# Kernel optimization log

Measured on AMD Instinct MI355X. Metric: run time of the kernel, lower is better.

## Reference

```python
import jax, jax.numpy as jnp
import numpy as np

N, C, H, W = 16, 64, 128, 128
SHIFT = 1  # frozen value of torch module's random.randint(-2, 2) drawn at __init__


def setup_inputs() -> dict:
    key = jax.random.key(0)
    k1, k2, k3 = jax.random.split(key, 3)
    x = jax.random.normal(k1, (N, C, H, W), dtype=jnp.float32)
    # p_3: Conv2d(c, c, (1,5), padding=(0,2), bias=False) -> weight (C_out, C_in, 1, 5)
    w3 = jax.random.normal(k2, (C, C, 1, 5), dtype=jnp.float32) * (1.0 / np.sqrt(5.0 * C))
    # p_7: Conv2d(9c, c, 1, groups=c, bias=False) -> per output channel, 9 input channels: (C, 9)
    w7 = jax.random.normal(k3, (C, 9), dtype=jnp.float32) * (1.0 / 3.0)
    return {"x": x, "w3": w3, "w7": w7}


def reference(x, w3, w7):
    n, c, h, w = x.shape
    # t_1: F.unfold(x, (1,3), dilation=(1,2), padding=(0,2)) -> width offsets -2, 0, +2 (zero padded)
    xp = jnp.pad(x, ((0, 0), (0, 0), (0, 0), (2, 2)))
    t1 = jnp.stack([xp[..., 0:w], xp[..., 2:w + 2], xp[..., 4:w + 4]], axis=2)  # (n,c,3,h,w)
    # t_3: 1x5 conv, padding (0,2)
    t3 = jax.lax.conv_general_dilated(
        x, w3, window_strides=(1, 1), padding=[(0, 0), (2, 2)],
        dimension_numbers=("NCHW", "OIHW", "NCHW"))  # (n,c,h,w)
    # t_4: F.unfold(t1 as (n,3c,h,w), (3,1), padding=(1,0)) -> height offsets -1, 0, +1
    t1p = jnp.pad(t1, ((0, 0), (0, 0), (0, 0), (1, 1), (0, 0)))
    t4 = jnp.stack([t1p[..., 0:h, :], t1p[..., 1:h + 1, :], t1p[..., 2:h + 2, :]],
                   axis=3)  # (n, c, 3[w_off], 3[h_off], h, w)
    # t_5: roll along the W axis (dim 5)
    t5 = jnp.roll(t4, SHIFT, axis=5)
    # t_6: maximum of lhs (n,c,1,3,h,w) and rhs (n,c,3,3,h,w); lhs offset dim aligns with rhs dim 3
    t6 = jnp.maximum(t1[:, :, None, :, :, :], t5)  # (n,c,3,3,h,w)
    # t_7: grouped 1x1 conv, groups=c, 9 input channels per group -> 1 output channel
    t6f = t6.reshape(n, c, 9, h, w)
    t7 = jnp.einsum("nckhw,ck->nchw", t6f, w7)
    return t7 * t3
```

## Files before the change

kernel.cpp:

```cpp
#include <hip/hip_runtime.h>

#define NN 16
#define CC 64
#define HH 128
#define WW 128

#define LDS_STRIDE 72
#define T3B_STRIDE 132

typedef __attribute__((ext_vector_type(8))) short short8;
typedef __attribute__((ext_vector_type(4))) float floatx4;

__device__ __forceinline__ short f2bf(float f) {
    union { float f; unsigned u; } v; v.f = f;
    unsigned r = v.u + 0x7fffu + ((v.u >> 16) & 1u);
    return (short)(r >> 16);
}
__device__ __forceinline__ unsigned pack2bf(float lo, float hi) {
    union { float f; unsigned u; } a, b; a.f = lo; b.f = hi;
    unsigned ra = a.u + 0x7fffu + ((a.u >> 16) & 1u);
    unsigned rb = b.u + 0x7fffu + ((b.u >> 16) & 1u);
    return (ra >> 16) | (rb & 0xffff0000u);
}
__device__ __forceinline__ float bf2f(unsigned short u) {
    union { unsigned u; float f; } v; v.u = ((unsigned)u) << 16;
    return v.f;
}

__global__ __launch_bounds__(256) void prep_w(const float* __restrict__ w3,
                                              short* __restrict__ Abf,
                                              float* __restrict__ zp) {
    int idx = blockIdx.x * 256 + threadIdx.x;
    if (idx < CC * CC * 5) {
        int tap = idx % 5;
        int ci  = (idx / 5) % CC;
        int co  = idx / (5 * CC);
        Abf[co * 320 + tap * 64 + ci] = f2bf(w3[idx]);
    }
    if (blockIdx.x == 0 && threadIdx.x < 64) zp[threadIdx.x] = 0.f;
}

__global__ __launch_bounds__(256, 4) void fused(const float* __restrict__ x,
                                                const short* __restrict__ Abf,
                                                const float* __restrict__ w7,
                                                const float* __restrict__ zp,
                                                float* __restrict__ out) {
    __shared__ __align__(16) char smem[132 * LDS_STRIDE * 2];
    short*    xsT = (short*)smem;
    unsigned* xsW = (unsigned*)smem;
    short*    t3b = (short*)smem;

    const int bid = blockIdx.x;
    const int nh  = ((bid & 7) << 8) | (bid >> 3);
    const int n   = nh >> 7;
    const int h   = nh & (HH - 1);
    const int tid = threadIdx.x;

    const float* xbase = x + (((size_t)n * CC) * HH + h) * WW;
    {
        const int cp  = tid & 31;
        const int wqg = tid >> 5;
        const float* r0 = xbase + (size_t)(2 * cp) * (HH * WW);
        const float* r1 = r0 + HH * WW;
        #pragma unroll
        for (int q = 0; q < 4; ++q) {
            int wq = wqg * 4 + q;
            float4 a = *(const float4*)(r0 + wq * 4);
            float4 b = *(const float4*)(r1 + wq * 4);
            int wp = wq * 4 + 2;
            xsW[(wp + 0) * 36 + cp] = pack2bf(a.x, b.x);
            xsW[(wp + 1) * 36 + cp] = pack2bf(a.y, b.y);
            xsW[(wp + 2) * 36 + cp] = pack2bf(a.z, b.z);
            xsW[(wp + 3) * 36 + cp] = pack2bf(a.w, b.w);
        }
        if (tid < 128) {
            int wpi = tid >> 5;
            int wpz = (wpi < 2) ? wpi : 128 + wpi;
            xsW[wpz * 36 + (tid & 31)] = 0u;
        }
    }
    __syncthreads();

    const int W    = tid >> 6;
    const int lane = tid & 63;
    const int lm   = lane & 15;
    const int g    = lane >> 4;

    floatx4 acc[8];
    #pragma unroll
    for (int nt = 0; nt < 8; ++nt) acc[nt] = (floatx4){0.f, 0.f, 0.f, 0.f};

    const short* arow = Abf + (W * 16 + lm) * 320;

    for (int ks = 0; ks < 10; ++ks) {
        const int kbase = ks * 32 + g * 8;
        const int tap   = kbase >> 6;
        const int cib   = kbase & 63;

        short8 a = *(const short8*)(arow + kbase);
        #pragma unroll
        for (int nt = 0; nt < 8; ++nt) {
            int wp = nt * 16 + lm + tap;
            short8 b = *(const short8*)&xsT[wp * LDS_STRIDE + cib];
            acc[nt] = __builtin_amdgcn_mfma_f32_16x16x32_bf16(a, b, acc[nt], 0, 0, 0);
        }
    }
    __syncthreads();

    #pragma unroll
    for (int nt = 0; nt < 8; ++nt) {
        #pragma unroll
        for (int r = 0; r < 4; ++r) {
            int co = W * 16 + g * 4 + r;
            t3b[co * T3B_STRIDE + nt * 16 + lm] = f2bf(acc[nt][r]);
        }
    }

    const int w0  = (tid & 31) * 4;
    const int chi = tid >> 5;
    const bool isw = (w0 == 0);
    const int src  = lane | 31;

    const float* p[9];
    int s[9];
    const float* xb0 = x + (((size_t)(n * CC + chi)) * HH) * WW;
    #pragma unroll
    for (int r = 0; r < 3; ++r) {
        int hh = h + r - 1;
        bool hok = (unsigned)hh < HH;
        #pragma unroll
        for (int q = 0; q < 3; ++q) {
            int cb = w0 - 4 + q * 4;
            bool ok = hok && (unsigned)cb < WW;
            p[r * 3 + q] = ok ? (xb0 + (size_t)hh * WW + cb) : zp;
            s[r * 3 + q] = ok ? (8 * HH * WW) : 0;
        }
    }
    const float* wcp = w7 + chi * 9;
    int t3o = chi * T3B_STRIDE + w0;
    float* outp = out + ((((size_t)(n * CC + chi)) * HH + h) * WW) + w0;

    float4 cur[9];
    #pragma unroll
    for (int t = 0; t < 9; ++t) { cur[t] = *(const float4*)p[t]; p[t] += s[t]; }

    __syncthreads();

    #pragma unroll
    for (int it = 0; it < 8; ++it) {
        float4 nxt[9];
        if (it < 7) {
            #pragma unroll
            for (int t = 0; t < 9; ++t) { nxt[t] = *(const float4*)p[t]; p[t] += s[t]; }
        }

        float win[3][12];
        #pragma unroll
        for (int r = 0; r < 3; ++r) {
            #pragma unroll
            for (int q = 0; q < 3; ++q) {
                float4 v = cur[r * 3 + q];
                win[r][q * 4 + 0] = v.x; win[r][q * 4 + 1] = v.y;
                win[r][q * 4 + 2] = v.z; win[r][q * 4 + 3] = v.w;
            }
        }
        float wrap0[3], wrap1[3];
        #pragma unroll
        for (int r = 0; r < 3; ++r) {
            wrap0[r] = __shfl(win[r][5], src);
            wrap1[r] = __shfl(win[r][7], src);
        }

        float wc[9];
        #pragma unroll
        for (int t = 0; t < 9; ++t) wc[t] = wcp[t];

        ushort4 tv = *(const ushort4*)&t3b[t3o];
        float t3v[4] = {bf2f(tv.x), bf2f(tv.y), bf2f(tv.z), bf2f(tv.w)};

        float res[4];
        #pragma unroll
        for (int e = 0; e < 4; ++e) {
            float a = 0.f;
            #pragma unroll
            for (int j = 0; j < 3; ++j) {
                #pragma unroll
                for (int i = 0; i < 3; ++i) {
                    float lhs = win[1][e + 2 * i + 2];
                    float rhs = win[i][e + 2 * j + 1];
                    if (e == 0)
                        rhs = isw ? ((j == 0) ? wrap0[i]
                                   : (j == 1) ? wrap1[i] : 0.f)
                                  : rhs;
                    a = fmaf(wc[j * 3 + i], fmaxf(lhs, rhs), a);
                }
            }
            res[e] = a;
        }
        float4 o;
        o.x = res[0] * t3v[0]; o.y = res[1] * t3v[1];
        o.z = res[2] * t3v[2]; o.w = res[3] * t3v[3];
        *(float4*)outp = o;

        wcp  += 8 * 9;
        t3o  += 8 * T3B_STRIDE;
        outp += (size_t)8 * HH * WW;
        #pragma unroll
        for (int t = 0; t < 9; ++t) cur[t] = nxt[t];
    }
}

extern "C" void kernel_launch(void* const* d_in, const int* in_sizes, int n_in,
                              void* d_out, int out_size, void* d_ws, size_t ws_size,
                              hipStream_t stream) {
    const float* x  = (const float*)d_in[0];
    const float* w3 = (const float*)d_in[1];
    const float* w7 = (const float*)d_in[2];
    float* out = (float*)d_out;

    short* Abf = (short*)d_ws;
    float* zp  = (float*)((char*)d_ws + 40960);

    prep_w<<<(CC * CC * 5 + 255) / 256, 256, 0, stream>>>(w3, Abf, zp);
    fused<<<NN * HH, 256, 0, stream>>>(x, Abf, w7, zp, out);
}
```

Before: 146.8 us.

## Use 512-thread blocks, separate LDS for conv result, stage w7 in LDS

```diff
diff --git a/kernel.cpp b/kernel.cpp
--- a/kernel.cpp
+++ b/kernel.cpp
@@ -28,8 +28,7 @@
 }
 
 __global__ __launch_bounds__(256) void prep_w(const float* __restrict__ w3,
-                                              short* __restrict__ Abf,
-                                              float* __restrict__ zp) {
+                                              short* __restrict__ Abf) {
     int idx = blockIdx.x * 256 + threadIdx.x;
     if (idx < CC * CC * 5) {
         int tap = idx % 5;
@@ -37,18 +36,17 @@
         int co  = idx / (5 * CC);
         Abf[co * 320 + tap * 64 + ci] = f2bf(w3[idx]);
     }
-    if (blockIdx.x == 0 && threadIdx.x < 64) zp[threadIdx.x] = 0.f;
-}
-
-__global__ __launch_bounds__(256, 4) void fused(const float* __restrict__ x,
+}
+
+__global__ __launch_bounds__(512, 8) void fused(const float* __restrict__ x,
                                                 const short* __restrict__ Abf,
                                                 const float* __restrict__ w7,
-                                                const float* __restrict__ zp,
                                                 float* __restrict__ out) {
-    __shared__ __align__(16) char smem[132 * LDS_STRIDE * 2];
+    __shared__ __align__(16) char smem[132 * LDS_STRIDE * 2 + CC * T3B_STRIDE * 2 + 768 * 4];
     short*    xsT = (short*)smem;
     unsigned* xsW = (unsigned*)smem;
-    short*    t3b = (short*)smem;
+    short*    t3b = (short*)(smem + 132 * LDS_STRIDE * 2);
+    float*    ws7 = (float*)(smem + 132 * LDS_STRIDE * 2 + CC * T3B_STRIDE * 2);
 
     const int bid = blockIdx.x;
     const int nh  = ((bid & 7) << 8) | (bid >> 3);
@@ -63,8 +61,8 @@
         const float* r0 = xbase + (size_t)(2 * cp) * (HH * WW);
         const float* r1 = r0 + HH * WW;
         #pragma unroll
-        for (int q = 0; q < 4; ++q) {
-            int wq = wqg * 4 + q;
+        for (int q = 0; q < 2; ++q) {
+            int wq = wqg * 2 + q;
             float4 a = *(const float4*)(r0 + wq * 4);
             float4 b = *(const float4*)(r1 + wq * 4);
             int wp = wq * 4 + 2;
@@ -78,19 +76,25 @@
             int wpz = (wpi < 2) ? wpi : 128 + wpi;
             xsW[wpz * 36 + (tid & 31)] = 0u;
         }
+        for (int i = tid; i < CC * 9; i += 512) {
+            int c = i / 9, j = i - c * 9;
+            ws7[c * 12 + j] = w7[i];
+        }
     }
     __syncthreads();
 
-    const int W    = tid >> 6;
+    const int wv   = tid >> 6;
     const int lane = tid & 63;
     const int lm   = lane & 15;
     const int g    = lane >> 4;
-
-    floatx4 acc[8];
-    #pragma unroll
-    for (int nt = 0; nt < 8; ++nt) acc[nt] = (floatx4){0.f, 0.f, 0.f, 0.f};
-
-    const short* arow = Abf + (W * 16 + lm) * 320;
+    const int ct   = wv & 3;
+    const int ntb  = (wv >> 2) * 4;
+
+    floatx4 acc[4];
+    #pragma unroll
+    for (int k = 0; k < 4; ++k) acc[k] = (floatx4){0.f, 0.f, 0.f, 0.f};
+
+    const short* arow = Abf + (ct * 16 + lm) * 320;
 
     for (int ks = 0; ks < 10; ++ks) {
         const int kbase = ks * 32 + g * 8;
@@ -99,70 +103,60 @@
 
         short8 a = *(const short8*)(arow + kbase);
         #pragma unroll
-        for (int nt = 0; nt < 8; ++nt) {
-            int wp = nt * 16 + lm + tap;
+        for (int k = 0; k < 4; ++k) {
+            int wp = (ntb + k) * 16 + lm + tap;
             short8 b = *(const short8*)&xsT[wp * LDS_STRIDE + cib];
-            acc[nt] = __builtin_amdgcn_mfma_f32_16x16x32_bf16(a, b, acc[nt], 0, 0, 0);
+            acc[k] = __builtin_amdgcn_mfma_f32_16x16x32_bf16(a, b, acc[k], 0, 0, 0);
+        }
+    }
+
+    #pragma unroll
+    for (int k = 0; k < 4; ++k) {
+        #pragma unroll
+        for (int r = 0; r < 4; ++r) {
+            int co = ct * 16 + g * 4 + r;
+            t3b[co * T3B_STRIDE + (ntb + k) * 16 + lm] = f2bf(acc[k][r]);
         }
     }
     __syncthreads();
 
-    #pragma unroll
-    for (int nt = 0; nt < 8; ++nt) {
-        #pragma unroll
-        for (int r = 0; r < 4; ++r) {
-            int co = W * 16 + g * 4 + r;
-            t3b[co * T3B_STRIDE + nt * 16 + lm] = f2bf(acc[nt][r]);
-        }
-    }
-
+    const int chi = tid >> 5;
     const int w0  = (tid & 31) * 4;
-    const int chi = tid >> 5;
-    const bool isw = (w0 == 0);
-    const int src  = lane | 31;
-
-    const float* p[9];
-    int s[9];
-    const float* xb0 = x + (((size_t)(n * CC + chi)) * HH) * WW;
+    const bool isw  = (w0 == 0);
+    const bool cok0 = (w0 > 0);
+    const bool cok2 = (w0 < 124);
+    const int  src  = lane | 31;
+    const int coff0 = cok0 ? (w0 - 4) : 0;
+    const int coff2 = cok2 ? (w0 + 4) : 124;
+
+    const float* rp[3];
+    bool hok[3];
     #pragma unroll
     for (int r = 0; r < 3; ++r) {
         int hh = h + r - 1;
-        bool hok = (unsigned)hh < HH;
-        #pragma unroll
-        for (int q = 0; q < 3; ++q) {
-            int cb = w0 - 4 + q * 4;
-            bool ok = hok && (unsigned)cb < WW;
-            p[r * 3 + q] = ok ? (xb0 + (size_t)hh * WW + cb) : zp;
-            s[r * 3 + q] = ok ? (8 * HH * WW) : 0;
-        }
-    }
-    const float* wcp = w7 + chi * 9;
+        hok[r] = (unsigned)hh < HH;
+        int hcl = hh < 0 ? 0 : (hh > HH - 1 ? HH - 1 : hh);
+        rp[r] = x + (((size_t)(n * CC + chi)) * HH + hcl) * WW;
+    }
+    float* outp = out + ((((size_t)(n * CC + chi)) * HH + h) * WW) + w0;
     int t3o = chi * T3B_STRIDE + w0;
-    float* outp = out + ((((size_t)(n * CC + chi)) * HH + h) * WW) + w0;
-
-    float4 cur[9];
-    #pragma unroll
-    for (int t = 0; t < 9; ++t) { cur[t] = *(const float4*)p[t]; p[t] += s[t]; }
-
-    __syncthreads();
-
-    #pragma unroll
-    for (int it = 0; it < 8; ++it) {
-        float4 nxt[9];
-        if (it < 7) {
-            #pragma unroll
-            for (int t = 0; t < 9; ++t) { nxt[t] = *(const float4*)p[t]; p[t] += s[t]; }
-        }
-
+    const float* wrow = ws7 + chi * 12;
+
+    #pragma unroll
+    for (int it = 0; it < 4; ++it) {
         float win[3][12];
         #pragma unroll
         for (int r = 0; r < 3; ++r) {
-            #pragma unroll
-            for (int q = 0; q < 3; ++q) {
-                float4 v = cur[r * 3 + q];
-                win[r][q * 4 + 0] = v.x; win[r][q * 4 + 1] = v.y;
-                win[r][q * 4 + 2] = v.z; win[r][q * 4 + 3] = v.w;
-            }
+            float4 v0 = *(const float4*)(rp[r] + coff0);
+            float4 v1 = *(const float4*)(rp[r] + w0);
+            float4 v2 = *(const float4*)(rp[r] + coff2);
+            bool m0 = hok[r] && cok0, m1 = hok[r], m2 = hok[r] && cok2;
+            win[r][0]  = m0 ? v0.x : 0.f; win[r][1]  = m0 ? v0.y : 0.f;
+            win[r][2]  = m0 ? v0.z : 0.f; win[r][3]  = m0 ? v0.w : 0.f;
+            win[r][4]  = m1 ? v1.x : 0.f; win[r][5]  = m1 ? v1.y : 0.f;
+            win[r][6]  = m1 ? v1.z : 0.f; win[r][7]  = m1 ? v1.w : 0.f;
+            win[r][8]  = m2 ? v2.x : 0.f; win[r][9]  = m2 ? v2.y : 0.f;
+            win[r][10] = m2 ? v2.z : 0.f; win[r][11] = m2 ? v2.w : 0.f;
         }
         float wrap0[3], wrap1[3];
         #pragma unroll
@@ -171,9 +165,10 @@
             wrap1[r] = __shfl(win[r][7], src);
         }
 
-        float wc[9];
-        #pragma unroll
-        for (int t = 0; t < 9; ++t) wc[t] = wcp[t];
+        float4 wca = *(const float4*)(wrow);
+        float4 wcb = *(const float4*)(wrow + 4);
+        float  wcl = wrow[8];
+        float wc[9] = {wca.x, wca.y, wca.z, wca.w, wcb.x, wcb.y, wcb.z, wcb.w, wcl};
 
         ushort4 tv = *(const ushort4*)&t3b[t3o];
         float t3v[4] = {bf2f(tv.x), bf2f(tv.y), bf2f(tv.z), bf2f(tv.w)};
@@ -202,11 +197,11 @@
         o.z = res[2] * t3v[2]; o.w = res[3] * t3v[3];
         *(float4*)outp = o;
 
-        wcp  += 8 * 9;
-        t3o  += 8 * T3B_STRIDE;
-        outp += (size_t)8 * HH * WW;
-        #pragma unroll
-        for (int t = 0; t < 9; ++t) cur[t] = nxt[t];
+        #pragma unroll
+        for (int r = 0; r < 3; ++r) rp[r] += (size_t)16 * HH * WW;
+        outp += (size_t)16 * HH * WW;
+        t3o  += 16 * T3B_STRIDE;
+        wrow += 16 * 12;
     }
 }
 
@@ -219,8 +214,7 @@
     float* out = (float*)d_out;
 
     short* Abf = (short*)d_ws;
-    float* zp  = (float*)((char*)d_ws + 40960);
-
-    prep_w<<<(CC * CC * 5 + 255) / 256, 256, 0, stream>>>(w3, Abf, zp);
-    fused<<<NN * HH, 256, 0, stream>>>(x, Abf, w7, zp, out);
-}
+
+    prep_w<<<(CC * CC * 5 + 255) / 256, 256, 0, stream>>>(w3, Abf);
+    fused<<<NN * HH, 512, 0, stream>>>(x, Abf, w7, out);
+}
```

Measured after the change: 199.9 us. 1.36x slower.

## Split conv MFMA into two halves to cut accumulators and raise occupancy

Applied to the files above, without the earlier changes.

```diff
diff --git a/kernel.cpp b/kernel.cpp
--- a/kernel.cpp
+++ b/kernel.cpp
@@ -6,7 +6,7 @@
 #define WW 128
 
 #define LDS_STRIDE 72
-#define T3B_STRIDE 132
+#define T3B_STRIDE 68
 
 typedef __attribute__((ext_vector_type(8))) short short8;
 typedef __attribute__((ext_vector_type(4))) float floatx4;
@@ -40,15 +40,16 @@
     if (blockIdx.x == 0 && threadIdx.x < 64) zp[threadIdx.x] = 0.f;
 }
 
-__global__ __launch_bounds__(256, 4) void fused(const float* __restrict__ x,
+__global__ __launch_bounds__(256, 8) void fused(const float* __restrict__ x,
                                                 const short* __restrict__ Abf,
                                                 const float* __restrict__ w7,
                                                 const float* __restrict__ zp,
                                                 float* __restrict__ out) {
     __shared__ __align__(16) char smem[132 * LDS_STRIDE * 2];
-    short*    xsT = (short*)smem;
-    unsigned* xsW = (unsigned*)smem;
-    short*    t3b = (short*)smem;
+    short*    xsT  = (short*)smem;
+    unsigned* xsW  = (unsigned*)smem;
+    short*    t3bA = (short*)smem;
+    short*    t3bB = (short*)(smem + 9216);
 
     const int bid = blockIdx.x;
     const int nh  = ((bid & 7) << 8) | (bid >> 3);
@@ -81,38 +82,61 @@
     }
     __syncthreads();
 
-    const int W    = tid >> 6;
+    const int wv   = tid >> 6;
     const int lane = tid & 63;
     const int lm   = lane & 15;
     const int g    = lane >> 4;
-
-    floatx4 acc[8];
-    #pragma unroll
-    for (int nt = 0; nt < 8; ++nt) acc[nt] = (floatx4){0.f, 0.f, 0.f, 0.f};
-
-    const short* arow = Abf + (W * 16 + lm) * 320;
-
+    const short* arow = Abf + (wv * 16 + lm) * 320;
+
+    floatx4 acc[4];
+
+    #pragma unroll
+    for (int k = 0; k < 4; ++k) acc[k] = (floatx4){0.f, 0.f, 0.f, 0.f};
     for (int ks = 0; ks < 10; ++ks) {
         const int kbase = ks * 32 + g * 8;
         const int tap   = kbase >> 6;
         const int cib   = kbase & 63;
-
         short8 a = *(const short8*)(arow + kbase);
         #pragma unroll
-        for (int nt = 0; nt < 8; ++nt) {
-            int wp = nt * 16 + lm + tap;
+        for (int k = 0; k < 4; ++k) {
+            int wp = k * 16 + lm + tap;
             short8 b = *(const short8*)&xsT[wp * LDS_STRIDE + cib];
-            acc[nt] = __builtin_amdgcn_mfma_f32_16x16x32_bf16(a, b, acc[nt], 0, 0, 0);
-        }
-    }
-    __syncthreads();
-
-    #pragma unroll
-    for (int nt = 0; nt < 8; ++nt) {
+            acc[k] = __builtin_amdgcn_mfma_f32_16x16x32_bf16(a, b, acc[k], 0, 0, 0);
+        }
+    }
+    __syncthreads();
+
+    #pragma unroll
+    for (int k = 0; k < 4; ++k) {
         #pragma unroll
         for (int r = 0; r < 4; ++r) {
-            int co = W * 16 + g * 4 + r;
-            t3b[co * T3B_STRIDE + nt * 16 + lm] = f2bf(acc[nt][r]);
+            int co = wv * 16 + g * 4 + r;
+            t3bA[co * T3B_STRIDE + k * 16 + lm] = f2bf(acc[k][r]);
+        }
+    }
+
+    #pragma unroll
+    for (int k = 0; k < 4; ++k) acc[k] = (floatx4){0.f, 0.f, 0.f, 0.f};
+    for (int ks = 0; ks < 10; ++ks) {
+        const int kbase = ks * 32 + g * 8;
+        const int tap   = kbase >> 6;
+        const int cib   = kbase & 63;
+        short8 a = *(const short8*)(arow + kbase);
+        #pragma unroll
+        for (int k = 0; k < 4; ++k) {
+            int wp = (k + 4) * 16 + lm + tap;
+            short8 b = *(const short8*)&xsT[wp * LDS_STRIDE + cib];
+            acc[k] = __builtin_amdgcn_mfma_f32_16x16x32_bf16(a, b, acc[k], 0, 0, 0);
+        }
+    }
+    __syncthreads();
+
+    #pragma unroll
+    for (int k = 0; k < 4; ++k) {
+        #pragma unroll
+        for (int r = 0; r < 4; ++r) {
+            int co = wv * 16 + g * 4 + r;
+            t3bB[co * T3B_STRIDE + k * 16 + lm] = f2bf(acc[k][r]);
         }
     }
 
@@ -137,7 +161,7 @@
         }
     }
     const float* wcp = w7 + chi * 9;
-    int t3o = chi * T3B_STRIDE + w0;
+    const short* t3p = (w0 < 64 ? t3bA + w0 : t3bB + (w0 - 64)) + chi * T3B_STRIDE;
     float* outp = out + ((((size_t)(n * CC + chi)) * HH + h) * WW) + w0;
 
     float4 cur[9];
@@ -175,7 +199,7 @@
         #pragma unroll
         for (int t = 0; t < 9; ++t) wc[t] = wcp[t];
 
-        ushort4 tv = *(const ushort4*)&t3b[t3o];
+        ushort4 tv = *(const ushort4*)t3p;
         float t3v[4] = {bf2f(tv.x), bf2f(tv.y), bf2f(tv.z), bf2f(tv.w)};
 
         float res[4];
@@ -203,7 +227,7 @@
         *(float4*)outp = o;
 
         wcp  += 8 * 9;
-        t3o  += 8 * T3B_STRIDE;
+        t3p  += 8 * T3B_STRIDE;
         outp += (size_t)8 * HH * WW;
         #pragma unroll
         for (int t = 0; t < 9; ++t) cur[t] = nxt[t];
```

After: 205.4 us. 1.4x slower.
